# Kernel optimization log

Measured on AMD Instinct MI355X. Metric: run time of the kernel, lower is better.

## Reference

```python
import jax, jax.numpy as jnp
import numpy as np

K = 20      # knn fan-in (constructor arg)
EPS = 1e-5  # LayerNorm eps (torch default)

def ln(x, g, b):
    m = jnp.mean(x, axis=-1, keepdims=True)
    v = jnp.mean((x - m) ** 2, axis=-1, keepdims=True)
    return (x - m) / jnp.sqrt(v + EPS) * g + b

def setup_inputs():
    key = jax.random.key(0)
    ks = jax.random.split(key, 12)
    N, Cin, Cout, H = 4096, 128, 128, 512
    def w(k, i, o):
        return (jax.random.normal(k, (i, o), jnp.float32) / np.sqrt(i)).astype(jnp.float32)
    return dict(
        x=jax.random.normal(ks[0], (N, Cin), jnp.float32),
        pos=jax.random.normal(ks[1], (N, 3), jnp.float32),
        batch=jnp.zeros((N,), jnp.int32),
        # PointTransformerConv linears (bias=False in PyG)
        W_lin=w(ks[2], Cin, Cout),
        W_src=w(ks[3], Cin, Cout),
        W_dst=w(ks[4], Cin, Cout),
        # pos_nn: Lin(3,H) LN ELU Lin(H,Cout) LN ELU
        pw1=w(ks[5], 3, H), pb1=jnp.zeros((H,), jnp.float32),
        pg1=jnp.ones((H,), jnp.float32), pbt1=jnp.zeros((H,), jnp.float32),
        pw2=w(ks[6], H, Cout), pb2=jnp.zeros((Cout,), jnp.float32),
        pg2=jnp.ones((Cout,), jnp.float32), pbt2=jnp.zeros((Cout,), jnp.float32),
        # attn_nn: Lin(Cout,H) LN ELU Lin(H,Cout) LN ELU
        aw1=w(ks[7], Cout, H), ab1=jnp.zeros((H,), jnp.float32),
        ag1=jnp.ones((H,), jnp.float32), abt1=jnp.zeros((H,), jnp.float32),
        aw2=w(ks[8], H, Cout), ab2=jnp.zeros((Cout,), jnp.float32),
        ag2=jnp.ones((Cout,), jnp.float32), abt2=jnp.zeros((Cout,), jnp.float32),
    )

def knn_idx(pos):
    # single-graph knn (batch is constant zero); returns [N, K+1] neighbor idx
    # with self-loop appended (PointTransformerConv add_self_loops=True).
    N = pos.shape[0]
    sq = jnp.sum(pos * pos, axis=1)
    d2 = sq[:, None] + sq[None, :] - 2.0 * (pos @ pos.T)      # [N, N]
    d2 = d2.at[jnp.arange(N), jnp.arange(N)].set(jnp.inf)      # loop=False
    _, nbr = jax.lax.top_k(-d2, K)                             # [N, K]
    return jnp.concatenate([nbr, jnp.arange(N)[:, None]], axis=1)

def reference(x, pos, batch, W_lin, W_src, W_dst,
              pw1, pb1, pg1, pbt1, pw2, pb2, pg2, pbt2,
              aw1, ab1, ag1, abt1, aw2, ab2, ag2, abt2):
    idx = knn_idx(pos)                      # [N, K+1] source node per edge
    v = x @ W_lin                           # message values
    a_src = x @ W_src
    a_dst = x @ W_dst
    rel = pos[:, None, :] - pos[idx]        # pos_i - pos_j, [N, K+1, 3]
    h = jax.nn.elu(ln(rel @ pw1 + pb1, pg1, pbt1))
    delta = jax.nn.elu(ln(h @ pw2 + pb2, pg2, pbt2))           # [N, K+1, C]
    alpha = a_dst[:, None, :] - a_src[idx] + delta
    h2 = jax.nn.elu(ln(alpha @ aw1 + ab1, ag1, abt1))
    alpha = jax.nn.elu(ln(h2 @ aw2 + ab2, ag2, abt2))
    alpha = jax.nn.softmax(alpha, axis=1)   # softmax over neighbors of i
    return jnp.sum(alpha * (v[idx] + delta), axis=1)           # [N, C]
```

## Files before the change

kernel.cpp:

```cpp
#include <hip/hip_runtime.h>
#include <math.h>

#define NN    4096
#define CIN   128
#define CO    128
#define HD    512
#define KK    20
#define EE    21
#define EDGES (NN * EE)
#define LNEPS 1e-5f

typedef unsigned short u16;
typedef unsigned int   u32;
typedef unsigned long long u64;
typedef __attribute__((ext_vector_type(8))) short bf16x8;
typedef __attribute__((ext_vector_type(4))) float f32x4;

#define MFMA16(a,b,c) __builtin_amdgcn_mfma_f32_16x16x32_bf16(a,b,c,0,0,0)

__device__ __forceinline__ u16 f2b(float x) {
    u32 u = __float_as_uint(x);
    u32 r = u + 0x7fffu + ((u >> 16) & 1u);
    return (u16)(r >> 16);
}
__device__ __forceinline__ float b2f(u16 h) {
    return __uint_as_float(((u32)h) << 16);
}

__global__ __launch_bounds__(64) void k_knn(const float* __restrict__ pos,
                                            int* __restrict__ idxg)
{
    int i = blockIdx.x;
    int lane = threadIdx.x;
    float px = pos[3*i], py = pos[3*i+1], pz = pos[3*i+2];
    float bd[KK]; int bi[KK];
#pragma unroll
    for (int s = 0; s < KK; ++s) { bd[s] = INFINITY; bi[s] = 0x7fffffff; }
    for (int j = lane; j < NN; j += 64) {
        float dx = px - pos[3*j], dy = py - pos[3*j+1], dz = pz - pos[3*j+2];
        float d2 = dx*dx + dy*dy + dz*dz;
        if (j != i && d2 < bd[KK-1]) {
            float cd = d2; int ci = j;
#pragma unroll
            for (int s = 0; s < KK; ++s) {
                bool sw = cd < bd[s];
                float td = sw ? bd[s] : cd;  int ti = sw ? bi[s] : ci;
                bd[s] = sw ? cd : bd[s];     bi[s] = sw ? ci : bi[s];
                cd = td; ci = ti;
            }
        }
    }
    for (int r = 0; r < KK; ++r) {
        u64 m = ~0ull;
#pragma unroll
        for (int s = 0; s < KK; ++s) {
            u64 k = ((u64)__float_as_uint(bd[s]) << 32) | (u32)bi[s];
            m = k < m ? k : m;
        }
#pragma unroll
        for (int off = 32; off > 0; off >>= 1) {
            u64 o = __shfl_xor(m, off, 64);
            m = o < m ? o : m;
        }
        if (lane == 0) idxg[i*EE + r] = (int)(u32)m;
#pragma unroll
        for (int s = 0; s < KK; ++s) {
            u64 k = ((u64)__float_as_uint(bd[s]) << 32) | (u32)bi[s];
            if (k == m) bd[s] = INFINITY;
        }
    }
    if (lane == 0) idxg[i*EE + KK] = i;
}

__global__ __launch_bounds__(256) void k_lin3(const float* __restrict__ x,
        const float* __restrict__ Wl, const float* __restrict__ Ws, const float* __restrict__ Wd,
        float* __restrict__ v, float* __restrict__ as_, float* __restrict__ ad)
{
    __shared__ float sx[8][CIN];
    int b = blockIdx.x, t = threadIdx.x;
    int n0 = b * 8;
    for (int q = t; q < 8*CIN; q += 256) sx[q >> 7][q & 127] = x[n0*CIN + q];
    __syncthreads();
    int c = t & 127, g = t >> 7;
    float al[4] = {0,0,0,0}, asr[4] = {0,0,0,0}, adr[4] = {0,0,0,0};
    for (int k = 0; k < CIN; ++k) {
        float wl = Wl[k*CO + c], ws = Ws[k*CO + c], wd = Wd[k*CO + c];
#pragma unroll
        for (int nn2 = 0; nn2 < 4; ++nn2) {
            float xv = sx[g*4 + nn2][k];
            al[nn2]  = fmaf(xv, wl, al[nn2]);
            asr[nn2] = fmaf(xv, ws, asr[nn2]);
            adr[nn2] = fmaf(xv, wd, adr[nn2]);
        }
    }
#pragma unroll
    for (int nn2 = 0; nn2 < 4; ++nn2) {
        int n = n0 + g*4 + nn2;
        v[n*CO + c]   = al[nn2];
        as_[n*CO + c] = asr[nn2];
        ad[n*CO + c]  = adr[nn2];
    }
}

__global__ __launch_bounds__(256) void k_wconv3(
        const float* __restrict__ aw1, const float* __restrict__ aw2,
        const float* __restrict__ pw2,
        u16* __restrict__ awp1, u16* __restrict__ awp2, u16* __restrict__ pwp2)
{
    int gb = blockIdx.x;
    const float* src; u16* dst; int N, kplog, base;
    if (gb < 256)      { src = aw1; dst = awp1; N = HD; kplog = 2; base = 0;   }
    else if (gb < 512) { src = aw2; dst = awp2; N = CO; kplog = 4; base = 256; }
    else               { src = pw2; dst = pwp2; N = CO; kplog = 4; base = 512; }
    int idx = (gb - base)*256 + threadIdx.x;
    int j  = idx & 7;
    int l  = (idx >> 3) & 63;
    int ks = (idx >> 9) & ((1 << kplog) - 1);
    int nt = idx >> (9 + kplog);
    int k = ks*32 + (l >> 4)*8 + j;
    int c = nt*16 + (l & 15);
    dst[idx] = f2b(src[(size_t)k*N + c]);
}

template<int L, int NW>
__device__ __forceinline__ void ln_elu_b16(u16* base, int rows, int stride,
        const float* __restrict__ gam, const float* __restrict__ bet)
{
    constexpr int P = L / 64;
    int t = threadIdx.x, lane = t & 63, w = t >> 6;
    float g[P], b[P];
#pragma unroll
    for (int q = 0; q < P; q += 4) {
        *(float4*)&g[q] = *(const float4*)&gam[lane*P + q];
        *(float4*)&b[q] = *(const float4*)&bet[lane*P + q];
    }
    for (int e = w; e < rows; e += NW) {
        u16* row = base + e*stride + lane*P;
        u16 raw[P];
        *(ushort4*)&raw[0] = *(const ushort4*)&row[0];
        *(ushort4*)&raw[4] = *(const ushort4*)&row[4];
        float vals[P]; float s = 0.f, sq = 0.f;
#pragma unroll
        for (int q = 0; q < P; ++q) {
            float xx = b2f(raw[q]);
            vals[q] = xx; s += xx; sq += xx*xx;
        }
#pragma unroll
        for (int off = 32; off > 0; off >>= 1) {
            s  += __shfl_xor(s,  off, 64);
            sq += __shfl_xor(sq, off, 64);
        }
        float mn = s * (1.0f / L);
        float rstd = rsqrtf(sq * (1.0f / L) - mn*mn + LNEPS);
#pragma unroll
        for (int q = 0; q < P; ++q) {
            float y = (vals[q] - mn) * rstd * g[q] + b[q];
            y = y > 0.f ? y : __expf(y) - 1.f;
            raw[q] = f2b(y);
        }
        *(ushort4*)&row[0] = *(const ushort4*)&raw[0];
        *(ushort4*)&row[4] = *(const ushort4*)&raw[4];
    }
}

template<int L, int NW>
__device__ __forceinline__ void ln_elu_f32v(float* base, int rows, int stride,
        const float* __restrict__ gam, const float* __restrict__ bet)
{
    constexpr int P = L / 64;
    int t = threadIdx.x, lane = t & 63, w = t >> 6;
    float g[P], b[P];
    *(float2*)&g[0] = *(const float2*)&gam[lane*P];
    *(float2*)&b[0] = *(const float2*)&bet[lane*P];
    for (int e = w; e < rows; e += NW) {
        float* row = base + e*stride + lane*P;
        float vals[P];
        *(float2*)&vals[0] = *(const float2*)&row[0];
        float s = 0.f, sq = 0.f;
#pragma unroll
        for (int q = 0; q < P; ++q) { s += vals[q]; sq += vals[q]*vals[q]; }
#pragma unroll
        for (int off = 32; off > 0; off >>= 1) {
            s  += __shfl_xor(s,  off, 64);
            sq += __shfl_xor(sq, off, 64);
        }
        float mn = s * (1.0f / L);
        float rstd = rsqrtf(sq * (1.0f / L) - mn*mn + LNEPS);
#pragma unroll
        for (int q = 0; q < P; ++q) {
            float y = (vals[q] - mn) * rstd * g[q] + b[q];
            vals[q] = y > 0.f ? y : __expf(y) - 1.f;
        }
        *(float2*)&row[0] = *(const float2*)&vals[0];
    }
}

#define SA_S 136
#define SH_S 520
#define SF_S 132

__global__ __launch_bounds__(512) void k_posnn(
        const float* __restrict__ pos, const int* __restrict__ idxg,
        const float* __restrict__ pw1, const float* __restrict__ pb1,
        const float* __restrict__ pg1, const float* __restrict__ pbt1,
        const u16* __restrict__ pwp2, const float* __restrict__ pb2,
        const float* __restrict__ pg2, const float* __restrict__ pbt2,
        u16* __restrict__ delta)
{
    __shared__ __align__(16) u16   s_h[32*SH_S];
    __shared__ __align__(16) float s_d[32*SF_S];
    __shared__ float s_rel[32][3];
    int t = threadIdx.x;
    int e0g = blockIdx.x * 32;
    if (t < 32) {
        int e = e0g + t;
        u32 ii = (u32)e / 21u;
        int j = idxg[e];
        s_rel[t][0] = pos[3*ii]   - pos[3*j];
        s_rel[t][1] = pos[3*ii+1] - pos[3*j+1];
        s_rel[t][2] = pos[3*ii+2] - pos[3*j+2];
    }
    __syncthreads();
    {
        int c1 = t;
        float wa0 = pw1[c1], wa1 = pw1[HD + c1], wa2 = pw1[2*HD + c1], ba = pb1[c1];
        for (int r = 0; r < 32; ++r) {
            float hv = fmaf(s_rel[r][2], wa2, fmaf(s_rel[r][1], wa1, fmaf(s_rel[r][0], wa0, ba)));
            s_h[r*SH_S + c1] = f2b(hv);
        }
    }
    __syncthreads();
    ln_elu_b16<HD, 8>(s_h, 32, SH_S, pg1, pbt1);
    __syncthreads();
    {
        int w = t >> 6, l = t & 63, lr = l & 15, lk = l >> 4;
        int m = w & 1, nt0 = (w >> 1) * 2;
        bf16x8 afr[16];
#pragma unroll
        for (int ks = 0; ks < 16; ++ks)
            afr[ks] = *(const bf16x8*)&s_h[(m*16 + lr)*SH_S + ks*32 + lk*8];
#pragma unroll
        for (int n2 = 0; n2 < 2; ++n2) {
            int nt = nt0 + n2;
            const u16* bp = pwp2 + ((size_t)nt*16*64 + l)*8;
            f32x4 acc = {0.f, 0.f, 0.f, 0.f};
#pragma unroll
            for (int ks = 0; ks < 16; ++ks) {
                bf16x8 bfr = *(const bf16x8*)(bp + ks*512);
                acc = MFMA16(afr[ks], bfr, acc);
            }
            float bias = pb2[nt*16 + lr];
#pragma unroll
            for (int r = 0; r < 4; ++r)
                s_d[(m*16 + lk*4 + r)*SF_S + nt*16 + lr] = acc[r] + bias;
        }
    }
    __syncthreads();
    ln_elu_f32v<CO, 8>(s_d, 32, SF_S, pg2, pbt2);
    __syncthreads();
    {
        int el = t >> 4, c0 = (t & 15) << 3;
        const float* sp = &s_d[el*SF_S + c0];
        float4 v0 = *(const float4*)(sp);
        float4 v1 = *(const float4*)(sp + 4);
        bf16x8 o;
        o[0] = (short)f2b(v0.x); o[1] = (short)f2b(v0.y);
        o[2] = (short)f2b(v0.z); o[3] = (short)f2b(v0.w);
        o[4] = (short)f2b(v1.x); o[5] = (short)f2b(v1.y);
        o[6] = (short)f2b(v1.z); o[7] = (short)f2b(v1.w);
        *(bf16x8*)&delta[(size_t)(e0g + el)*CO + c0] = o;
    }
}

__global__ __launch_bounds__(512) void k_amlp(
        const int* __restrict__ idxg,
        const float* __restrict__ as_, const float* __restrict__ ad,
        const u16* __restrict__ delta,
        const u16* __restrict__ awp1, const float* __restrict__ ab1,
        const float* __restrict__ ag1, const float* __restrict__ abt1,
        const u16* __restrict__ awp2, const float* __restrict__ ab2,
        const float* __restrict__ ag2, const float* __restrict__ abt2,
        u16* __restrict__ alphaF)
{
    __shared__ __align__(16) u16   s_a[32*SA_S];
    __shared__ __align__(16) u16   s_h[32*SH_S];
    __shared__ __align__(16) float s_af[32*SF_S];
    int t = threadIdx.x;
    int e0g = blockIdx.x * 32;
    {
        int el = t >> 4, c0 = (t & 15) << 3;
        int e = e0g + el;
        int i = (int)((u32)e / 21u);
        int j = idxg[e];
        const float* adp = ad  + i*CIN + c0;
        const float* asp = as_ + j*CIN + c0;
        const u16*  dp   = delta + (size_t)e*CO + c0;
        float4 a0 = *(const float4*)(adp);
        float4 a1 = *(const float4*)(adp + 4);
        float4 s0 = *(const float4*)(asp);
        float4 s1 = *(const float4*)(asp + 4);
        bf16x8 d8 = *(const bf16x8*)(dp);
        bf16x8 o;
        o[0] = (short)f2b(a0.x - s0.x + b2f((u16)d8[0]));
        o[1] = (short)f2b(a0.y - s0.y + b2f((u16)d8[1]));
        o[2] = (short)f2b(a0.z - s0.z + b2f((u16)d8[2]));
        o[3] = (short)f2b(a0.w - s0.w + b2f((u16)d8[3]));
        o[4] = (short)f2b(a1.x - s1.x + b2f((u16)d8[4]));
        o[5] = (short)f2b(a1.y - s1.y + b2f((u16)d8[5]));
        o[6] = (short)f2b(a1.z - s1.z + b2f((u16)d8[6]));
        o[7] = (short)f2b(a1.w - s1.w + b2f((u16)d8[7]));
        *(bf16x8*)&s_a[el*SA_S + c0] = o;
    }
    __syncthreads();
    int w = t >> 6, l = t & 63, lr = l & 15, lk = l >> 4;
    {
        int m = w & 1, nt0 = (w >> 1) * 8;
        bf16x8 afr[4];
#pragma unroll
        for (int ks = 0; ks < 4; ++ks)
            afr[ks] = *(const bf16x8*)&s_a[(m*16 + lr)*SA_S + ks*32 + lk*8];
#pragma unroll
        for (int n2 = 0; n2 < 8; ++n2) {
            int nt = nt0 + n2;
            const u16* bp = awp1 + ((size_t)nt*4*64 + l)*8;
            f32x4 acc = {0.f, 0.f, 0.f, 0.f};
#pragma unroll
            for (int ks = 0; ks < 4; ++ks) {
                bf16x8 bfr = *(const bf16x8*)(bp + ks*512);
                acc = MFMA16(afr[ks], bfr, acc);
            }
            float bias = ab1[nt*16 + lr];
#pragma unroll
            for (int r = 0; r < 4; ++r)
                s_h[(m*16 + lk*4 + r)*SH_S + nt*16 + lr] = f2b(acc[r] + bias);
        }
    }
    __syncthreads();
    ln_elu_b16<HD, 8>(s_h, 32, SH_S, ag1, abt1);
    __syncthreads();
    {
        int m = w & 1, nt0 = (w >> 1) * 2;
        bf16x8 afr[16];
#pragma unroll
        for (int ks = 0; ks < 16; ++ks)
            afr[ks] = *(const bf16x8*)&s_h[(m*16 + lr)*SH_S + ks*32 + lk*8];
#pragma unroll
        for (int n2 = 0; n2 < 2; ++n2) {
            int nt = nt0 + n2;
            const u16* bp = awp2 + ((size_t)nt*16*64 + l)*8;
            f32x4 acc = {0.f, 0.f, 0.f, 0.f};
#pragma unroll
            for (int ks = 0; ks < 16; ++ks) {
                bf16x8 bfr = *(const bf16x8*)(bp + ks*512);
                acc = MFMA16(afr[ks], bfr, acc);
            }
            float bias = ab2[nt*16 + lr];
#pragma unroll
            for (int r = 0; r < 4; ++r)
                s_af[(m*16 + lk*4 + r)*SF_S + nt*16 + lr] = acc[r] + bias;
        }
    }
    __syncthreads();
    ln_elu_f32v<CO, 8>(s_af, 32, SF_S, ag2, abt2);
    __syncthreads();
    {
        int el = t >> 4, c0 = (t & 15) << 3;
        const float* sp = &s_af[el*SF_S + c0];
        float4 v0 = *(const float4*)(sp);
        float4 v1 = *(const float4*)(sp + 4);
        bf16x8 o;
        o[0] = (short)f2b(v0.x); o[1] = (short)f2b(v0.y);
        o[2] = (short)f2b(v0.z); o[3] = (short)f2b(v0.w);
        o[4] = (short)f2b(v1.x); o[5] = (short)f2b(v1.y);
        o[6] = (short)f2b(v1.z); o[7] = (short)f2b(v1.w);
        *(bf16x8*)&alphaF[(size_t)(e0g + el)*CO + c0] = o;
    }
}

__global__ __launch_bounds__(256) void k_agg(
        const int* __restrict__ idxg,
        const float* __restrict__ v, const u16* __restrict__ delta,
        const u16* __restrict__ alphaF, float* __restrict__ out)
{
    __shared__ int s_idx[8][EE];
    int b = blockIdx.x, t = threadIdx.x;
    int n0 = b * 8;
    for (int q = t; q < 8*EE; q += 256) s_idx[q/EE][q%EE] = idxg[n0*EE + q];
    __syncthreads();
    int c = t & 127, g = t >> 7;
    for (int ng = g; ng < 8; ng += 2) {
        int i = n0 + ng;
        size_t base = (size_t)i*EE*CO + c;
        float af[EE]; float mx = -INFINITY;
#pragma unroll
        for (int e = 0; e < EE; ++e) { af[e] = b2f(alphaF[base + e*CO]); mx = fmaxf(mx, af[e]); }
        float ssum = 0.f;
#pragma unroll
        for (int e = 0; e < EE; ++e) { af[e] = __expf(af[e] - mx); ssum += af[e]; }
        float accv = 0.f;
#pragma unroll
        for (int e = 0; e < EE; ++e) {
            int j = s_idx[ng][e];
            float msg = v[j*CO + c] + b2f(delta[base + e*CO]);
            accv = fmaf(af[e], msg, accv);
        }
        out[i*CO + c] = accv / ssum;
    }
}

extern "C" void kernel_launch(void* const* d_in, const int* in_sizes, int n_in,
                              void* d_out, int out_size, void* d_ws, size_t ws_size,
                              hipStream_t stream)
{
    const float* x    = (const float*)d_in[0];
    const float* pos  = (const float*)d_in[1];
    const float* Wl   = (const float*)d_in[3];
    const float* Wsrc = (const float*)d_in[4];
    const float* Wdst = (const float*)d_in[5];
    const float* pw1  = (const float*)d_in[6];
    const float* pb1  = (const float*)d_in[7];
    const float* pg1  = (const float*)d_in[8];
    const float* pbt1 = (const float*)d_in[9];
    const float* pw2  = (const float*)d_in[10];
    const float* pb2  = (const float*)d_in[11];
    const float* pg2  = (const float*)d_in[12];
    const float* pbt2 = (const float*)d_in[13];
    const float* aw1  = (const float*)d_in[14];
    const float* ab1  = (const float*)d_in[15];
    const float* ag1  = (const float*)d_in[16];
    const float* abt1 = (const float*)d_in[17];
    const float* aw2  = (const float*)d_in[18];
    const float* ab2  = (const float*)d_in[19];
    const float* ag2  = (const float*)d_in[20];
    const float* abt2 = (const float*)d_in[21];
    float* out = (float*)d_out;

    char* ws = (char*)d_ws;
    int*   idxg   = (int*)ws;
    u16*   awp1   = (u16*)(ws + 0x54000);
    u16*   awp2   = (u16*)(ws + 0x74000);
    u16*   pwp2   = (u16*)(ws + 0x94000);
    float* v      = (float*)(ws + 0xC0000);
    float* asrc   = (float*)(ws + 0x2C0000);
    float* adst   = (float*)(ws + 0x4C0000);
    u16*   delta  = (u16*)(ws + 0x6C0000);
    u16*   alphaF = (u16*)(ws + 0x6C0000 + 0x1500000);

    k_knn   <<<NN,       64,  0, stream>>>(pos, idxg);
    k_wconv3<<<768,      256, 0, stream>>>(aw1, aw2, pw2, awp1, awp2, pwp2);
    k_lin3  <<<NN/8,     256, 0, stream>>>(x, Wl, Wsrc, Wdst, v, asrc, adst);
    k_posnn <<<EDGES/32, 512, 0, stream>>>(pos, idxg, pw1, pb1, pg1, pbt1,
                                           pwp2, pb2, pg2, pbt2, delta);
    k_amlp  <<<EDGES/32, 512, 0, stream>>>(idxg, asrc, adst, delta,
                                           awp1, ab1, ag1, abt1,
                                           awp2, ab2, ag2, abt2, alphaF);
    k_agg   <<<NN/8,     256, 0, stream>>>(idxg, v, delta, alphaF, out);
}
```

Baseline: 292.0 us.

## Split second-layer MLP weights into hi/lo bf16 pairs and widen aggregation grid

The 512-to-128 weights of pos_nn and attn_nn are now stored as a bf16 high part plus a bf16 residual, and each MFMA step is issued twice to recover near-fp32 weight precision. This doubles the MFMA count and weight loads in those GEMMs, mainly to improve accuracy. The LayerNorm helpers are rewritten with explicit fmaf. k_agg now handles 2 nodes per block instead of 8, launching 4x more blocks for more parallelism. Workspace offsets are shifted to make room for the residual weights.

```diff
diff --git a/kernel.cpp b/kernel.cpp
--- a/kernel.cpp
+++ b/kernel.cpp
@@ -9,6 +9,7 @@
 #define EE    21
 #define EDGES (NN * EE)
 #define LNEPS 1e-5f
+#define WSZ   65536
 
 typedef unsigned short u16;
 typedef unsigned int   u32;
@@ -108,10 +109,10 @@
         u16* __restrict__ awp1, u16* __restrict__ awp2, u16* __restrict__ pwp2)
 {
     int gb = blockIdx.x;
-    const float* src; u16* dst; int N, kplog, base;
-    if (gb < 256)      { src = aw1; dst = awp1; N = HD; kplog = 2; base = 0;   }
-    else if (gb < 512) { src = aw2; dst = awp2; N = CO; kplog = 4; base = 256; }
-    else               { src = pw2; dst = pwp2; N = CO; kplog = 4; base = 512; }
+    const float* src; u16* dst; int N, kplog, base; bool split;
+    if (gb < 256)      { src = aw1; dst = awp1; N = HD; kplog = 2; base = 0;   split = false; }
+    else if (gb < 512) { src = aw2; dst = awp2; N = CO; kplog = 4; base = 256; split = true;  }
+    else               { src = pw2; dst = pwp2; N = CO; kplog = 4; base = 512; split = true;  }
     int idx = (gb - base)*256 + threadIdx.x;
     int j  = idx & 7;
     int l  = (idx >> 3) & 63;
@@ -119,7 +120,10 @@
     int nt = idx >> (9 + kplog);
     int k = ks*32 + (l >> 4)*8 + j;
     int c = nt*16 + (l & 15);
-    dst[idx] = f2b(src[(size_t)k*N + c]);
+    float w = src[(size_t)k*N + c];
+    u16 hi = f2b(w);
+    dst[idx] = hi;
+    if (split) dst[idx + WSZ] = f2b(w - b2f(hi));
 }
 
 template<int L, int NW>
@@ -143,7 +147,7 @@
 #pragma unroll
         for (int q = 0; q < P; ++q) {
             float xx = b2f(raw[q]);
-            vals[q] = xx; s += xx; sq += xx*xx;
+            vals[q] = xx; s += xx; sq = fmaf(xx, xx, sq);
         }
 #pragma unroll
         for (int off = 32; off > 0; off >>= 1) {
@@ -151,10 +155,13 @@
             sq += __shfl_xor(sq, off, 64);
         }
         float mn = s * (1.0f / L);
-        float rstd = rsqrtf(sq * (1.0f / L) - mn*mn + LNEPS);
+        float msq = mn * mn;
+        float var = fmaf(sq, 1.0f / L, -msq);
+        float rstd = rsqrtf(var + LNEPS);
 #pragma unroll
         for (int q = 0; q < P; ++q) {
-            float y = (vals[q] - mn) * rstd * g[q] + b[q];
+            float z = (vals[q] - mn) * rstd;
+            float y = fmaf(z, g[q], b[q]);
             y = y > 0.f ? y : __expf(y) - 1.f;
             raw[q] = f2b(y);
         }
@@ -178,17 +185,20 @@
         *(float2*)&vals[0] = *(const float2*)&row[0];
         float s = 0.f, sq = 0.f;
 #pragma unroll
-        for (int q = 0; q < P; ++q) { s += vals[q]; sq += vals[q]*vals[q]; }
+        for (int q = 0; q < P; ++q) { s += vals[q]; sq = fmaf(vals[q], vals[q], sq); }
 #pragma unroll
         for (int off = 32; off > 0; off >>= 1) {
             s  += __shfl_xor(s,  off, 64);
             sq += __shfl_xor(sq, off, 64);
         }
         float mn = s * (1.0f / L);
-        float rstd = rsqrtf(sq * (1.0f / L) - mn*mn + LNEPS);
+        float msq = mn * mn;
+        float var = fmaf(sq, 1.0f / L, -msq);
+        float rstd = rsqrtf(var + LNEPS);
 #pragma unroll
         for (int q = 0; q < P; ++q) {
-            float y = (vals[q] - mn) * rstd * g[q] + b[q];
+            float z = (vals[q] - mn) * rstd;
+            float y = fmaf(z, g[q], b[q]);
             vals[q] = y > 0.f ? y : __expf(y) - 1.f;
         }
         *(float2*)&row[0] = *(const float2*)&vals[0];
@@ -242,12 +252,15 @@
 #pragma unroll
         for (int n2 = 0; n2 < 2; ++n2) {
             int nt = nt0 + n2;
-            const u16* bp = pwp2 + ((size_t)nt*16*64 + l)*8;
+            const u16* bp  = pwp2 + ((size_t)nt*16*64 + l)*8;
+            const u16* bpl = bp + WSZ;
             f32x4 acc = {0.f, 0.f, 0.f, 0.f};
 #pragma unroll
             for (int ks = 0; ks < 16; ++ks) {
-                bf16x8 bfr = *(const bf16x8*)(bp + ks*512);
-                acc = MFMA16(afr[ks], bfr, acc);
+                bf16x8 bh = *(const bf16x8*)(bp + ks*512);
+                acc = MFMA16(afr[ks], bh, acc);
+                bf16x8 bl = *(const bf16x8*)(bpl + ks*512);
+                acc = MFMA16(afr[ks], bl, acc);
             }
             float bias = pb2[nt*16 + lr];
 #pragma unroll
@@ -347,12 +360,15 @@
 #pragma unroll
         for (int n2 = 0; n2 < 2; ++n2) {
             int nt = nt0 + n2;
-            const u16* bp = awp2 + ((size_t)nt*16*64 + l)*8;
+            const u16* bp  = awp2 + ((size_t)nt*16*64 + l)*8;
+            const u16* bpl = bp + WSZ;
             f32x4 acc = {0.f, 0.f, 0.f, 0.f};
 #pragma unroll
             for (int ks = 0; ks < 16; ++ks) {
-                bf16x8 bfr = *(const bf16x8*)(bp + ks*512);
-                acc = MFMA16(afr[ks], bfr, acc);
+                bf16x8 bh = *(const bf16x8*)(bp + ks*512);
+                acc = MFMA16(afr[ks], bh, acc);
+                bf16x8 bl = *(const bf16x8*)(bpl + ks*512);
+                acc = MFMA16(afr[ks], bl, acc);
             }
             float bias = ab2[nt*16 + lr];
 #pragma unroll
@@ -382,30 +398,28 @@
         const float* __restrict__ v, const u16* __restrict__ delta,
         const u16* __restrict__ alphaF, float* __restrict__ out)
 {
-    __shared__ int s_idx[8][EE];
+    __shared__ int s_idx[2][EE];
     int b = blockIdx.x, t = threadIdx.x;
-    int n0 = b * 8;
-    for (int q = t; q < 8*EE; q += 256) s_idx[q/EE][q%EE] = idxg[n0*EE + q];
+    int n0 = b * 2;
+    if (t < 2*EE) s_idx[t/EE][t%EE] = idxg[n0*EE + t];
     __syncthreads();
     int c = t & 127, g = t >> 7;
-    for (int ng = g; ng < 8; ng += 2) {
-        int i = n0 + ng;
-        size_t base = (size_t)i*EE*CO + c;
-        float af[EE]; float mx = -INFINITY;
-#pragma unroll
-        for (int e = 0; e < EE; ++e) { af[e] = b2f(alphaF[base + e*CO]); mx = fmaxf(mx, af[e]); }
-        float ssum = 0.f;
-#pragma unroll
-        for (int e = 0; e < EE; ++e) { af[e] = __expf(af[e] - mx); ssum += af[e]; }
-        float accv = 0.f;
-#pragma unroll
-        for (int e = 0; e < EE; ++e) {
-            int j = s_idx[ng][e];
-            float msg = v[j*CO + c] + b2f(delta[base + e*CO]);
-            accv = fmaf(af[e], msg, accv);
-        }
-        out[i*CO + c] = accv / ssum;
-    }
+    int i = n0 + g;
+    size_t base = (size_t)i*EE*CO + c;
+    float af[EE]; float mx = -INFINITY;
+#pragma unroll
+    for (int e = 0; e < EE; ++e) { af[e] = b2f(alphaF[base + e*CO]); mx = fmaxf(mx, af[e]); }
+    float ssum = 0.f;
+#pragma unroll
+    for (int e = 0; e < EE; ++e) { af[e] = __expf(af[e] - mx); ssum += af[e]; }
+    float accv = 0.f;
+#pragma unroll
+    for (int e = 0; e < EE; ++e) {
+        int j = s_idx[g][e];
+        float msg = v[j*CO + c] + b2f(delta[base + e*CO]);
+        accv = fmaf(af[e], msg, accv);
+    }
+    out[i*CO + c] = accv / ssum;
 }
 
 extern "C" void kernel_launch(void* const* d_in, const int* in_sizes, int n_in,
@@ -439,12 +453,12 @@
     int*   idxg   = (int*)ws;
     u16*   awp1   = (u16*)(ws + 0x54000);
     u16*   awp2   = (u16*)(ws + 0x74000);
-    u16*   pwp2   = (u16*)(ws + 0x94000);
-    float* v      = (float*)(ws + 0xC0000);
-    float* asrc   = (float*)(ws + 0x2C0000);
-    float* adst   = (float*)(ws + 0x4C0000);
-    u16*   delta  = (u16*)(ws + 0x6C0000);
-    u16*   alphaF = (u16*)(ws + 0x6C0000 + 0x1500000);
+    u16*   pwp2   = (u16*)(ws + 0xB4000);
+    float* v      = (float*)(ws + 0x100000);
+    float* asrc   = (float*)(ws + 0x300000);
+    float* adst   = (float*)(ws + 0x500000);
+    u16*   delta  = (u16*)(ws + 0x700000);
+    u16*   alphaF = (u16*)(ws + 0x700000 + 0x1500000);
 
     k_knn   <<<NN,       64,  0, stream>>>(pos, idxg);
     k_wconv3<<<768,      256, 0, stream>>>(aw1, aw2, pw2, awp1, awp2, pwp2);
@@ -454,5 +468,5 @@
     k_amlp  <<<EDGES/32, 512, 0, stream>>>(idxg, asrc, adst, delta,
                                            awp1, ab1, ag1, abt1,
                                            awp2, ab2, ag2, abt2, alphaF);
-    k_agg   <<<NN/8,     256, 0, stream>>>(idxg, v, delta, alphaF, out);
-}
+    k_agg   <<<NN/2,     256, 0, stream>>>(idxg, v, delta, alphaF, out);
+}
```

Measured after the change: 327.5 us. 12.2% more time.
